# Optimization experiments

Hardware: AMD Instinct MI355X
Metric: run time of the kernel (lower is better)

## Reference

```python
import jax, jax.numpy as jnp
import numpy as np

D_IN = 768
D_SAE = 768 * 16  # expansion_factor = 16
K = 64
BATCH = 8192


def setup_inputs() -> dict:
    key = jax.random.key(0)
    k1, k2, k3 = jax.random.split(key, 3)
    x = jax.random.normal(k1, (BATCH, D_IN), dtype=jnp.float32)
    # Kaiming-uniform-ish encoder init (exact init values don't matter for correctness)
    bound = (6.0 / D_IN) ** 0.5
    W_enc = jax.random.uniform(k2, (D_IN, D_SAE), dtype=jnp.float32, minval=-bound, maxval=bound)
    b_enc = jnp.zeros((D_SAE,), dtype=jnp.float32)
    W_dec = jax.random.normal(k3, (D_SAE, D_IN), dtype=jnp.float32) * (1.0 / D_IN ** 0.5)
    # unit-norm decoder rows (per the module's normalize_decoder_weights)
    W_dec = W_dec / (jnp.linalg.norm(W_dec, axis=1, keepdims=True) + 1e-8)
    b_dec = jnp.zeros((D_IN,), dtype=jnp.float32)
    return {"x": x, "W_enc": W_enc, "b_enc": b_enc, "W_dec": W_dec, "b_dec": b_dec}


def reference(x, W_enc, b_enc, W_dec, b_dec):
    # encode: center, dense matmul, ReLU
    pre_acts = jax.nn.relu((x - b_dec) @ W_enc + b_enc)  # [B, d_sae]
    # top-k selection per row, scatter back into dense sparse_acts
    topk_vals, topk_idx = jax.lax.top_k(pre_acts, K)  # [B, K]
    rows = jnp.arange(pre_acts.shape[0])[:, None]  # [B, 1]
    sparse_acts = jnp.zeros_like(pre_acts).at[rows, topk_idx].set(topk_vals)
    # decode: dense matmul + bias
    reconstruction = sparse_acts @ W_dec + b_dec  # [B, d_in]
    return (reconstruction, sparse_acts)
```

## Files before the change

### kernel.cpp

```cpp
#include <hip/hip_runtime.h>
#include <hip/hip_fp16.h>
#include <stdint.h>

#define D_IN   768
#define D_SAE  12288
#define BATCH  8192
#define K_TOP  64
#define CAND_MAX 256


typedef _Float16 f16;
typedef _Float16 v8h __attribute__((ext_vector_type(8)));
typedef float v4f __attribute__((ext_vector_type(4)));

__device__ inline void async16(const void* g, void* l) {
    __builtin_amdgcn_global_load_lds(
        (const __attribute__((address_space(1))) unsigned int*)g,
        (__attribute__((address_space(3))) unsigned int*)l, 16, 0, 0);
}

__global__ __launch_bounds__(256) void k_convert_x(
    const float* __restrict__ x, const float* __restrict__ b_dec,
    f16* __restrict__ xhi)
{
    int i4 = (blockIdx.x * 256 + threadIdx.x) * 4;
    float4 v = *(const float4*)(x + i4);
    int col = i4 % D_IN;
    float vv[4] = { v.x - b_dec[col], v.y - b_dec[col + 1],
                    v.z - b_dec[col + 2], v.w - b_dec[col + 3] };
    union { short4 s; f16 h[4]; } H;
#pragma unroll
    for (int u = 0; u < 4; ++u) H.h[u] = (f16)vv[u];
    *(short4*)(xhi + i4) = H.s;
}

__global__ __launch_bounds__(256) void k_convert_wt(
    const float* __restrict__ W, f16* __restrict__ whiT, f16* __restrict__ wloT)
{
    __shared__ float tile[32][33];
    const int n0 = blockIdx.x * 32;
    const int k0 = blockIdx.y * 32;
    const int c = threadIdx.x & 31;
    const int rr = threadIdx.x >> 5;
#pragma unroll
    for (int s = 0; s < 4; ++s) {
        int r = s * 8 + rr;
        tile[r][c] = W[(size_t)(k0 + r) * D_SAE + n0 + c];
    }
    __syncthreads();
#pragma unroll
    for (int s = 0; s < 4; ++s) {
        int r2 = s * 8 + rr;
        float v = tile[c][r2];
        f16 hi = (f16)v;
        f16 lo = (f16)(v - (float)hi);
        whiT[(size_t)(n0 + r2) * D_IN + k0 + c] = hi;
        wloT[(size_t)(n0 + r2) * D_IN + k0 + c] = lo;
    }
}

__global__ __launch_bounds__(256) void k_convert_wd(
    const float* __restrict__ W, f16* __restrict__ Wh)
{
    int i4 = (blockIdx.x * 256 + threadIdx.x) * 4;
    float4 v = *(const float4*)(W + i4);
    union { short4 s; f16 h[4]; } H;
    H.h[0] = (f16)v.x; H.h[1] = (f16)v.y; H.h[2] = (f16)v.z; H.h[3] = (f16)v.w;
    *(short4*)(Wh + i4) = H.s;
}

__global__ __launch_bounds__(256) void k_gemm_f16(
    const f16* __restrict__ A,
    const f16* __restrict__ Bt,
    const float* __restrict__ b_enc,
    f16* __restrict__ outap)
{
    __shared__ union {
        struct { f16 A[2][128 * 32]; f16 B[2][128 * 32]; } ab;
        f16 C[128 * 136];
    } sm;
    const int tid  = threadIdx.x;
    const int wave = tid >> 6;
    const int lane = tid & 63;

    const int lid = blockIdx.y * 96 + blockIdx.x;
    const int xcd = lid & 7;
    const int idx = lid >> 3;
    const int sbx = xcd * 12 + (idx % 12);
    const int sby = idx / 12;
    const int bn = sbx * 128;
    const int bm = sby * 128;

    const int r16  = lane >> 2;
    const int kc8  = (lane & 3) * 8;
    const int mrow = lane & 15;
    const int quad = lane >> 4;
    const int wm = (wave & 1) * 64;
    const int wn = (wave >> 1) * 64;

    v4f acc[4][4] = {};

    const f16* gA = A  + (size_t)(bm + wave * 32 + r16) * D_IN + kc8;
    const f16* gB = Bt + (size_t)(bn + wave * 32 + r16) * D_IN + kc8;
    f16* lA0  = &sm.ab.A[0][(wave * 32) * 32];
    f16* lA0b = &sm.ab.A[0][(wave * 32 + 16) * 32];
    f16* lB0  = &sm.ab.B[0][(wave * 32) * 32];
    f16* lB0b = &sm.ab.B[0][(wave * 32 + 16) * 32];
    f16* lA1  = &sm.ab.A[1][(wave * 32) * 32];
    f16* lA1b = &sm.ab.A[1][(wave * 32 + 16) * 32];
    f16* lB1  = &sm.ab.B[1][(wave * 32) * 32];
    f16* lB1b = &sm.ab.B[1][(wave * 32 + 16) * 32];

    for (int k0 = 0; k0 < D_IN; k0 += 64) {
        __syncthreads();
        async16(gA + k0,               lA0);
        async16(gA + k0 + 16 * D_IN,   lA0b);
        async16(gB + k0,               lB0);
        async16(gB + k0 + 16 * D_IN,   lB0b);
        async16(gA + k0 + 32,              lA1);
        async16(gA + k0 + 32 + 16 * D_IN,  lA1b);
        async16(gB + k0 + 32,              lB1);
        async16(gB + k0 + 32 + 16 * D_IN,  lB1b);
        __syncthreads();

#pragma unroll
        for (int s = 0; s < 2; ++s) {
            v8h af[4], bf[4];
#pragma unroll
            for (int i = 0; i < 4; ++i)
                af[i] = *(const v8h*)&sm.ab.A[s][(wm + i * 16 + mrow) * 32 + quad * 8];
#pragma unroll
            for (int j = 0; j < 4; ++j)
                bf[j] = *(const v8h*)&sm.ab.B[s][(wn + j * 16 + mrow) * 32 + quad * 8];
#pragma unroll
            for (int i = 0; i < 4; ++i)
#pragma unroll
                for (int j = 0; j < 4; ++j)
                    acc[i][j] = __builtin_amdgcn_mfma_f32_16x16x32_f16(af[i], bf[j], acc[i][j], 0, 0, 0);
        }
    }

    __syncthreads();
#pragma unroll
    for (int i = 0; i < 4; ++i)
#pragma unroll
        for (int j = 0; j < 4; ++j)
#pragma unroll
            for (int r = 0; r < 4; ++r) {
                int lrow = wm + i * 16 + quad * 4 + r;
                int lcol = wn + j * 16 + mrow;
                float val = acc[i][j][r] + b_enc[bn + lcol];
                sm.C[lrow * 136 + lcol] = (f16)(val > 0.f ? val : 0.f);
            }
    __syncthreads();
    {
        const int r0 = tid >> 4;
        const int c8 = (tid & 15) * 8;
#pragma unroll
        for (int q = 0; q < 8; ++q) {
            int lrow = r0 + q * 16;
            v8h v = *(const v8h*)&sm.C[lrow * 136 + c8];
            __builtin_nontemporal_store(v,
                (v8h*)(outap + (size_t)(bm + lrow) * (2 * D_SAE) + bn + c8));
        }
    }
}

__device__ __forceinline__ unsigned suffix_scan_256(unsigned h, int t, unsigned* wtot, unsigned* tot_out) {
    const int lane = t & 63;
    const int w = t >> 6;
    unsigned s = h;
#pragma unroll
    for (int off = 1; off < 64; off <<= 1) {
        unsigned o = __shfl_down(s, off);
        if (lane + off < 64) s += o;
    }
    if (lane == 0) wtot[w] = s;
    __syncthreads();
    unsigned suf = s;
    unsigned tot = 0;
#pragma unroll
    for (int w2 = 0; w2 < 4; ++w2) {
        tot += wtot[w2];
        if (w2 > w) suf += wtot[w2];
    }
    *tot_out = tot;
    return suf;
}

__global__ __launch_bounds__(256) void k_topk2(
    float* __restrict__ sparse,
    const float* __restrict__ x,
    const f16* __restrict__ WhiT, const f16* __restrict__ WloT,
    const float* __restrict__ b_enc,
    const f16* __restrict__ Wdh,
    const float* __restrict__ b_dec,
    float* __restrict__ recon)
{
    const int row = blockIdx.x;
    const int t = threadIdx.x;
    const int lane = t & 63;
    float* rp = sparse + (size_t)row * D_SAE;
    const f16* ap = (const f16*)rp;

    v8h av[6];
#pragma unroll
    for (int j = 0; j < 6; ++j)
        av[j] = __builtin_nontemporal_load((const v8h*)(ap + ((size_t)j * 256 + t) * 8));

    __shared__ unsigned hist[256];
    __shared__ unsigned wtot[4];
    __shared__ float sh_cutoff;
    __shared__ int sh_ncand;
    __shared__ int   cand_i[CAND_MAX];
    __shared__ float cand_v[CAND_MAX];
    __shared__ float kept_v[K_TOP];
    __shared__ int   kept_i[K_TOP];
    __shared__ float xr[D_IN];
    __shared__ float wstage[64][67];

    const float margin = 0.05f;

    hist[t] = 0;
    if (t == 0) sh_ncand = 0;
    for (int k = t; k < D_IN; k += 256)
        xr[k] = x[(size_t)row * D_IN + k] - b_dec[k];
    __syncthreads();

#pragma unroll
    for (int j = 0; j < 6; ++j)
#pragma unroll
        for (int u = 0; u < 8; ++u) {
            float x0 = (float)av[j][u];
            if (x0 >= 2.0f) {
                int b = (int)((x0 - 2.0f) * 32.0f); if (b > 255) b = 255;
                atomicAdd(&hist[b], 1u);
            }
        }
    __syncthreads();
    unsigned h0 = hist[t];
    unsigned tot0;
    unsigned suf0 = suffix_scan_256(h0, t, wtot, &tot0);
    if (tot0 >= K_TOP) {
        if (suf0 >= K_TOP && suf0 - h0 < K_TOP)
            sh_cutoff = fmaxf(2.0f + (float)t * (1.0f / 32.0f) - margin, 1e-30f);
    }
    __syncthreads();
    if (tot0 < K_TOP) {
        hist[t] = 0;
        __syncthreads();
#pragma unroll
        for (int j = 0; j < 6; ++j)
#pragma unroll
            for (int u = 0; u < 8; ++u) {
                float x0 = (float)av[j][u];
                if (x0 >= 0.25f) {
                    int b = (int)(x0 * 32.0f); if (b > 255) b = 255;
                    atomicAdd(&hist[b], 1u);
                }
            }
        __syncthreads();
        unsigned h1 = hist[t];
        unsigned tot1;
        unsigned suf1 = suffix_scan_256(h1, t, wtot, &tot1);
        if (tot1 >= K_TOP) {
            if (suf1 >= K_TOP && suf1 - h1 < K_TOP)
                sh_cutoff = fmaxf((float)t * (1.0f / 32.0f) - margin, 1e-30f);
        }
        __syncthreads();
        if (tot1 < K_TOP) {
            hist[t] = 0;
            __syncthreads();
#pragma unroll
            for (int j = 0; j < 6; ++j)
#pragma unroll
                for (int u = 0; u < 8; ++u) {
                    float x0 = (float)av[j][u];
                    if (x0 > 0.0f && x0 < 0.25f) {
                        int b = (int)(x0 * 1024.0f); if (b > 255) b = 255;
                        atomicAdd(&hist[b], 1u);
                    }
                }
            __syncthreads();
            unsigned h2 = hist[t];
            unsigned tot2;
            unsigned suf2 = suffix_scan_256(h2, t, wtot, &tot2);
            unsigned need = K_TOP - tot1;
            if (tot2 >= need) {
                if (suf2 >= need && suf2 - h2 < need)
                    sh_cutoff = fmaxf((float)t * (1.0f / 1024.0f) - margin, 1e-30f);
            } else {
                if (t == 0) sh_cutoff = 1e-30f;
            }
        }
    }
    __syncthreads();
    const float cutoff = sh_cutoff;

#pragma unroll
    for (int j = 0; j < 6; ++j)
#pragma unroll
        for (int u = 0; u < 8; ++u) {
            float x0 = (float)av[j][u];
            bool pass = (x0 >= cutoff);
            unsigned long long m = __ballot(pass);
            if (m != 0ull) {
                int leader = (int)__builtin_ctzll(m);
                int cnt = (int)__builtin_popcountll(m);
                int base0 = 0;
                if (lane == leader) base0 = atomicAdd(&sh_ncand, cnt);
                base0 = __shfl(base0, leader);
                if (pass) {
                    int pos = base0 + (int)__builtin_popcountll(m & ((1ull << lane) - 1ull));
                    if (pos < CAND_MAX) { cand_i[pos] = (j * 256 + t) * 8 + u; cand_v[pos] = x0; }
                }
            }
        }
    __syncthreads();
    int ncand = sh_ncand; if (ncand > CAND_MAX) ncand = CAND_MAX;

    for (int cb = 0; cb < ncand; cb += 64) {
        float acc = 0.f;
        const int c = cb + t;
        const bool act = (t < 64) && (c < ncand);
        for (int kc = 0; kc < D_IN; kc += 64) {
            __syncthreads();
#pragma unroll
            for (int pass = 0; pass < 2; ++pass) {
                int rr = pass * 32 + (t >> 3);
                int e8 = (t & 7) * 8;
                if (cb + rr < ncand) {
                    const f16* wh = WhiT + (size_t)cand_i[cb + rr] * D_IN + kc + e8;
                    const f16* wl = WloT + (size_t)cand_i[cb + rr] * D_IN + kc + e8;
                    v8h hv = *(const v8h*)wh;
                    v8h lv = *(const v8h*)wl;
#pragma unroll
                    for (int u = 0; u < 8; ++u)
                        wstage[rr][e8 + u] = (float)hv[u] + (float)lv[u];
                }
            }
            __syncthreads();
            if (act) {
#pragma unroll
                for (int kk = 0; kk < 64; ++kk)
                    acc += xr[kc + kk] * wstage[t][kk];
            }
        }
        if (act) {
            acc += b_enc[cand_i[c]];
            cand_v[c] = acc > 0.f ? acc : 0.f;
        }
    }
    __syncthreads();

    for (int c = t; c < ncand; c += 256) {
        float vc = cand_v[c]; int ic = cand_i[c];
        int r = 0;
        for (int m = 0; m < ncand; ++m) {
            float vm = cand_v[m];
            r += (vm > vc || (vm == vc && cand_i[m] < ic)) ? 1 : 0;
        }
        if (r < K_TOP) { kept_v[r] = vc; kept_i[r] = ic; }
    }
    __syncthreads();
    int nk = ncand < K_TOP ? ncand : K_TOP;

#pragma unroll
    for (int j = 0; j < 12; ++j) {
        v4f z = {0.f, 0.f, 0.f, 0.f};
        __builtin_nontemporal_store(z, (v4f*)(rp + ((size_t)j * 256 + t) * 4));
    }
    __syncthreads();
    if (t < nk) rp[kept_i[t]] = kept_v[t];

    float r0 = b_dec[t], r1 = b_dec[t + 256], r2 = b_dec[t + 512];
#pragma unroll 4
    for (int m = 0; m < nk; ++m) {
        float val = kept_v[m];
        const f16* wr = Wdh + (size_t)kept_i[m] * D_IN;
        r0 += val * (float)wr[t];
        r1 += val * (float)wr[t + 256];
        r2 += val * (float)wr[t + 512];
    }
    float* rc = recon + (size_t)row * D_IN;
    __builtin_nontemporal_store(r0, rc + t);
    __builtin_nontemporal_store(r1, rc + t + 256);
    __builtin_nontemporal_store(r2, rc + t + 512);
}

extern "C" void kernel_launch(void* const* d_in, const int* in_sizes, int n_in,
                              void* d_out, int out_size, void* d_ws, size_t ws_size,
                              hipStream_t stream) {
    const float* x     = (const float*)d_in[0];
    const float* W_enc = (const float*)d_in[1];
    const float* b_enc = (const float*)d_in[2];
    const float* W_dec = (const float*)d_in[3];
    const float* b_dec = (const float*)d_in[4];
    float* out    = (float*)d_out;
    float* recon  = out;
    float* sparse = out + (size_t)BATCH * D_IN;

    const size_t xplane = (size_t)BATCH * D_IN;
    const size_t wplane = (size_t)D_SAE * D_IN;
    f16* xhi    = (f16*)d_ws;
    f16* whiT   = xhi + xplane;
    f16* wloT   = whiT + wplane;
    f16* wdh    = wloT + wplane;

    k_convert_x<<<xplane / 1024, 256, 0, stream>>>(x, b_dec, xhi);
    k_convert_wt<<<dim3(D_SAE / 32, D_IN / 32), 256, 0, stream>>>(W_enc, whiT, wloT);
    k_convert_wd<<<wplane / 1024, 256, 0, stream>>>(W_dec, wdh);
    k_gemm_f16<<<dim3(96, 64), 256, 0, stream>>>(xhi, whiT, b_enc, (f16*)sparse);
    k_topk2<<<BATCH, 256, 0, stream>>>(sparse, x, whiT, wloT, b_enc, wdh, b_dec, recon);
}
```

Baseline: 1.129 ms.

## Emit per-row candidate lists above threshold from GEMM epilogue for top-k

The GEMM epilogue now atomically appends every activation at or above 2.5 into a per-row (value, index) list, stored in the unused second half of each sparse output row, with a counter in the row's last word. The top-k kernel builds its histogram and candidate set from this short list instead of scanning all 12288 half-precision activations, and falls back to the full scan when the list is too short, overflows, or the chosen cutoff bin is too low. This is meant to cut the read and histogram cost of top-k. In exchange it adds global atomics in the GEMM epilogue, scattered 8-byte writes, and an extra launch to zero the counters.

Result: slower. 1.413 ms (+25.2%).

```diff
diff --git a/kernel.cpp b/kernel.cpp
--- a/kernel.cpp
+++ b/kernel.cpp
@@ -7,6 +7,8 @@
 #define BATCH  8192
 #define K_TOP  64
 #define CAND_MAX 256
+#define CAP    3000
+#define LIST_THR 2.5f
 
 
 typedef _Float16 f16;
@@ -17,6 +19,12 @@
     __builtin_amdgcn_global_load_lds(
         (const __attribute__((address_space(1))) unsigned int*)g,
         (__attribute__((address_space(3))) unsigned int*)l, 16, 0, 0);
+}
+
+__global__ __launch_bounds__(256) void k_zero_cnt(float* __restrict__ sparse)
+{
+    int row = blockIdx.x * 256 + threadIdx.x;
+    *(unsigned*)(sparse + (size_t)row * D_SAE + (D_SAE - 1)) = 0u;
 }
 
 __global__ __launch_bounds__(256) void k_convert_x(
@@ -151,6 +159,15 @@
                 int lcol = wn + j * 16 + mrow;
                 float val = acc[i][j][r] + b_enc[bn + lcol];
                 sm.C[lrow * 136 + lcol] = (f16)(val > 0.f ? val : 0.f);
+                if (val >= LIST_THR) {
+                    int grow = bm + lrow;
+                    float* orow = (float*)outap + (size_t)grow * D_SAE;
+                    unsigned pos = atomicAdd((unsigned*)(orow + (D_SAE - 1)), 1u);
+                    if (pos < CAP) {
+                        uint2 pr; pr.x = __float_as_uint(val); pr.y = (unsigned)(bn + lcol);
+                        ((uint2*)(orow + (D_SAE / 2)))[pos] = pr;
+                    }
+                }
             }
     __syncthreads();
     {
@@ -202,16 +219,13 @@
     const int lane = t & 63;
     float* rp = sparse + (size_t)row * D_SAE;
     const f16* ap = (const f16*)rp;
-
-    v8h av[6];
-#pragma unroll
-    for (int j = 0; j < 6; ++j)
-        av[j] = __builtin_nontemporal_load((const v8h*)(ap + ((size_t)j * 256 + t) * 8));
+    const uint2* lst = (const uint2*)(rp + (D_SAE / 2));
 
     __shared__ unsigned hist[256];
     __shared__ unsigned wtot[4];
     __shared__ float sh_cutoff;
-    __shared__ int sh_ncand;
+    __shared__ int   sh_bin;
+    __shared__ int   sh_ncand;
     __shared__ int   cand_i[CAND_MAX];
     __shared__ float cand_v[CAND_MAX];
     __shared__ float kept_v[K_TOP];
@@ -222,100 +236,123 @@
     const float margin = 0.05f;
 
     hist[t] = 0;
-    if (t == 0) sh_ncand = 0;
+    if (t == 0) { sh_ncand = 0; sh_bin = -1; }
     for (int k = t; k < D_IN; k += 256)
         xr[k] = x[(size_t)row * D_IN + k] - b_dec[k];
-    __syncthreads();
-
-#pragma unroll
-    for (int j = 0; j < 6; ++j)
-#pragma unroll
-        for (int u = 0; u < 8; ++u) {
-            float x0 = (float)av[j][u];
-            if (x0 >= 2.0f) {
-                int b = (int)((x0 - 2.0f) * 32.0f); if (b > 255) b = 255;
-                atomicAdd(&hist[b], 1u);
-            }
-        }
-    __syncthreads();
-    unsigned h0 = hist[t];
-    unsigned tot0;
-    unsigned suf0 = suffix_scan_256(h0, t, wtot, &tot0);
-    if (tot0 >= K_TOP) {
-        if (suf0 >= K_TOP && suf0 - h0 < K_TOP)
-            sh_cutoff = fmaxf(2.0f + (float)t * (1.0f / 32.0f) - margin, 1e-30f);
-    }
-    __syncthreads();
-    if (tot0 < K_TOP) {
+    const unsigned nl = *(const unsigned*)(rp + (D_SAE - 1));
+    bool fb = (nl < K_TOP) || (nl > CAP);
+    __syncthreads();
+
+    if (!fb) {
+        for (int c = t; c < (int)nl; c += 256) {
+            float v = __uint_as_float(lst[c].x);
+            int b = (int)((v - LIST_THR) * 32.0f);
+            if (b > 255) b = 255; if (b < 0) b = 0;
+            atomicAdd(&hist[b], 1u);
+        }
+        __syncthreads();
+        unsigned h0 = hist[t];
+        unsigned tot0;
+        unsigned suf0 = suffix_scan_256(h0, t, wtot, &tot0);
+        if (tot0 >= K_TOP) {
+            if (suf0 >= K_TOP && suf0 - h0 < K_TOP) {
+                sh_bin = t;
+                sh_cutoff = fmaxf(LIST_THR + (float)t * (1.0f / 32.0f) - margin, 1e-30f);
+            }
+        }
+        __syncthreads();
+        fb = (sh_bin < 2);
+    }
+
+    if (fb) {
         hist[t] = 0;
         __syncthreads();
-#pragma unroll
-        for (int j = 0; j < 6; ++j)
-#pragma unroll
-            for (int u = 0; u < 8; ++u) {
-                float x0 = (float)av[j][u];
-                if (x0 >= 0.25f) {
-                    int b = (int)(x0 * 32.0f); if (b > 255) b = 255;
-                    atomicAdd(&hist[b], 1u);
-                }
-            }
-        __syncthreads();
-        unsigned h1 = hist[t];
-        unsigned tot1;
-        unsigned suf1 = suffix_scan_256(h1, t, wtot, &tot1);
-        if (tot1 >= K_TOP) {
-            if (suf1 >= K_TOP && suf1 - h1 < K_TOP)
-                sh_cutoff = fmaxf((float)t * (1.0f / 32.0f) - margin, 1e-30f);
-        }
-        __syncthreads();
-        if (tot1 < K_TOP) {
+        for (int e = t; e < D_SAE; e += 256) {
+            float v = (float)ap[e];
+            if (v >= 2.0f) { int b = (int)((v - 2.0f) * 32.0f); if (b > 255) b = 255; atomicAdd(&hist[b], 1u); }
+        }
+        __syncthreads();
+        unsigned h0 = hist[t];
+        unsigned tot0;
+        unsigned suf0 = suffix_scan_256(h0, t, wtot, &tot0);
+        if (tot0 >= K_TOP) {
+            if (suf0 >= K_TOP && suf0 - h0 < K_TOP)
+                sh_cutoff = fmaxf(2.0f + (float)t * (1.0f / 32.0f) - margin, 1e-30f);
+        }
+        __syncthreads();
+        if (tot0 < K_TOP) {
             hist[t] = 0;
             __syncthreads();
-#pragma unroll
-            for (int j = 0; j < 6; ++j)
-#pragma unroll
-                for (int u = 0; u < 8; ++u) {
-                    float x0 = (float)av[j][u];
-                    if (x0 > 0.0f && x0 < 0.25f) {
-                        int b = (int)(x0 * 1024.0f); if (b > 255) b = 255;
-                        atomicAdd(&hist[b], 1u);
-                    }
-                }
+            for (int e = t; e < D_SAE; e += 256) {
+                float v = (float)ap[e];
+                if (v >= 0.25f) { int b = (int)(v * 32.0f); if (b > 255) b = 255; atomicAdd(&hist[b], 1u); }
+            }
             __syncthreads();
-            unsigned h2 = hist[t];
-            unsigned tot2;
-            unsigned suf2 = suffix_scan_256(h2, t, wtot, &tot2);
-            unsigned need = K_TOP - tot1;
-            if (tot2 >= need) {
-                if (suf2 >= need && suf2 - h2 < need)
-                    sh_cutoff = fmaxf((float)t * (1.0f / 1024.0f) - margin, 1e-30f);
-            } else {
-                if (t == 0) sh_cutoff = 1e-30f;
-            }
-        }
-    }
-    __syncthreads();
-    const float cutoff = sh_cutoff;
-
-#pragma unroll
-    for (int j = 0; j < 6; ++j)
-#pragma unroll
-        for (int u = 0; u < 8; ++u) {
-            float x0 = (float)av[j][u];
-            bool pass = (x0 >= cutoff);
+            unsigned h1 = hist[t];
+            unsigned tot1;
+            unsigned suf1 = suffix_scan_256(h1, t, wtot, &tot1);
+            if (tot1 >= K_TOP) {
+                if (suf1 >= K_TOP && suf1 - h1 < K_TOP)
+                    sh_cutoff = fmaxf((float)t * (1.0f / 32.0f) - margin, 1e-30f);
+            }
+            __syncthreads();
+            if (tot1 < K_TOP) {
+                hist[t] = 0;
+                __syncthreads();
+                for (int e = t; e < D_SAE; e += 256) {
+                    float v = (float)ap[e];
+                    if (v > 0.0f && v < 0.25f) { int b = (int)(v * 1024.0f); if (b > 255) b = 255; atomicAdd(&hist[b], 1u); }
+                }
+                __syncthreads();
+                unsigned h2 = hist[t];
+                unsigned tot2;
+                unsigned suf2 = suffix_scan_256(h2, t, wtot, &tot2);
+                unsigned need = K_TOP - tot1;
+                if (tot2 >= need) {
+                    if (suf2 >= need && suf2 - h2 < need)
+                        sh_cutoff = fmaxf((float)t * (1.0f / 1024.0f) - margin, 1e-30f);
+                } else {
+                    if (t == 0) sh_cutoff = 1e-30f;
+                }
+            }
+        }
+        __syncthreads();
+        const float cutoff = sh_cutoff;
+        for (int e = t; e < D_SAE; e += 256) {
+            float v = (float)ap[e];
+            bool pass = (v >= cutoff);
             unsigned long long m = __ballot(pass);
             if (m != 0ull) {
                 int leader = (int)__builtin_ctzll(m);
-                int cnt = (int)__builtin_popcountll(m);
+                int cn = (int)__builtin_popcountll(m);
                 int base0 = 0;
-                if (lane == leader) base0 = atomicAdd(&sh_ncand, cnt);
+                if (lane == leader) base0 = atomicAdd(&sh_ncand, cn);
                 base0 = __shfl(base0, leader);
                 if (pass) {
                     int pos = base0 + (int)__builtin_popcountll(m & ((1ull << lane) - 1ull));
-                    if (pos < CAND_MAX) { cand_i[pos] = (j * 256 + t) * 8 + u; cand_v[pos] = x0; }
-                }
-            }
-        }
+                    if (pos < CAND_MAX) { cand_i[pos] = e; cand_v[pos] = v; }
+                }
+            }
+        }
+    } else {
+        const float cutoff = sh_cutoff;
+        for (int c = t; c < (int)nl; c += 256) {
+            float v = __uint_as_float(lst[c].x);
+            bool pass = (v >= cutoff);
+            unsigned long long m = __ballot(pass);
+            if (m != 0ull) {
+                int leader = (int)__builtin_ctzll(m);
+                int cn = (int)__builtin_popcountll(m);
+                int base0 = 0;
+                if (lane == leader) base0 = atomicAdd(&sh_ncand, cn);
+                base0 = __shfl(base0, leader);
+                if (pass) {
+                    int pos = base0 + (int)__builtin_popcountll(m & ((1ull << lane) - 1ull));
+                    if (pos < CAND_MAX) { cand_i[pos] = (int)lst[c].y; cand_v[pos] = v; }
+                }
+            }
+        }
+    }
     __syncthreads();
     int ncand = sh_ncand; if (ncand > CAND_MAX) ncand = CAND_MAX;
 
@@ -407,6 +444,7 @@
     f16* wloT   = whiT + wplane;
     f16* wdh    = wloT + wplane;
 
+    k_zero_cnt<<<BATCH / 256, 256, 0, stream>>>(sparse);
     k_convert_x<<<xplane / 1024, 256, 0, stream>>>(x, b_dec, xhi);
     k_convert_wt<<<dim3(D_SAE / 32, D_IN / 32), 256, 0, stream>>>(W_enc, whiT, wloT);
     k_convert_wd<<<wplane / 1024, 256, 0, stream>>>(W_dec, wdh);
```
